# Kernel optimization log

Hardware: AMD Instinct MI355X
Metric: run time of the kernel (lower is better)

## Reference

```python
import jax, jax.numpy as jnp
import numpy as np

HOP = 2
N_NODES = 50000
D_FEAT = 64
N_NNZ = 800000
N_QEDGES = 32768


def setup_inputs() -> dict:
    key = jax.random.key(0)
    k1, k2, k3, k4, k5 = jax.random.split(key, 5)
    x = jax.random.normal(k1, (N_NODES, D_FEAT), dtype=jnp.float32)
    # degrees must be strictly positive (reciprocal / rsqrt / sqrt applied)
    deg = 1.0 + 63.0 * jax.random.uniform(k2, (N_NODES, 1), dtype=jnp.float32)
    adj_row = jnp.sort(jax.random.randint(k3, (N_NNZ,), 0, N_NODES, dtype=jnp.int32))
    adj_col = jax.random.randint(k4, (N_NNZ,), 0, N_NODES, dtype=jnp.int32)
    edge = jax.random.randint(k5, (2, N_QEDGES), 0, N_NODES, dtype=jnp.int32)
    return {"x": x, "deg": deg, "adj_row": adj_row, "adj_col": adj_col, "edge": edge}


def reference(x, deg, adj_row, adj_col, edge):
    N, D = x.shape
    degrev = 1.0 / deg                      # [N,1]
    # fused degree feature expansion: [N, 3D]
    x3 = jnp.concatenate((x, x * jax.lax.rsqrt(deg), x * jnp.sqrt(deg)), axis=1)

    def spmm(v):  # unweighted adj_t @ v via gather + segment-sum
        return jax.ops.segment_sum(v[adj_col], adj_row, num_segments=N)

    xs = [x3, degrev * spmm(x3)]
    for _ in range(2, HOP + 1):  # Chebyshev-like recurrence
        xs.append(degrev * spmm(xs[-1]) - xs[-2])
    h = jnp.concatenate(xs, axis=1)              # [N, (hop+1)*3*D]
    h = h.reshape(N, 3 * (HOP + 1), D)           # unflatten(1, (-1, D))
    h = jnp.transpose(h, (0, 2, 1))              # [N, D, 3*(hop+1)]
    return h[edge]                               # [2, E_q, D, 3*(hop+1)]
```

## Files before the change

kernel.cpp:

```cpp
#include <hip/hip_runtime.h>

#define N_NODES 50000
#define D_FEAT 64
#define N_NNZ 800000
#define N_ENT 65536

__global__ void build_rowptr_scal(const int* __restrict__ adj_row,
                                  const float* __restrict__ deg,
                                  int* __restrict__ row_ptr,
                                  float4* __restrict__ scal,
                                  int nnz, int n) {
    int r = blockIdx.x * blockDim.x + threadIdx.x;
    if (r > n) return;
    int lo = 0, hi = nnz;
    while (lo < hi) {
        int mid = (lo + hi) >> 1;
        if (adj_row[mid] < r) lo = mid + 1; else hi = mid;
    }
    row_ptr[r] = lo;
    if (r < n) {
        float d  = deg[r];
        float sq = sqrtf(d);
        scal[r] = make_float4(1.0f / d, 1.0f / sq, sq, 0.0f);
    }
}

__global__ __launch_bounds__(256) void spmm1_kernel(
    const float4* __restrict__ x4, const float4* __restrict__ scal,
    const int* __restrict__ adj_col, const int* __restrict__ row_ptr,
    float4* __restrict__ y1, int n) {
    int wave = threadIdx.x >> 6;
    int t    = threadIdx.x & 63;
    int sub  = t >> 4;
    int f    = t & 15;
    int r    = blockIdx.x * 4 + wave;
    if (r >= n) return;

    int s = row_ptr[r], e = row_ptr[r + 1];
    int cnt = e - s;
    float4 a0 = make_float4(0.f, 0.f, 0.f, 0.f), a1 = a0, a2 = a0;

    int nfull = cnt & ~3;
#pragma unroll 2
    for (int i = 0; i < nfull; i += 4) {
        int c = adj_col[s + i + sub];
        float4 sc = scal[c];
        float4 xv = x4[(size_t)c * 16 + f];
        a0.x += xv.x;        a0.y += xv.y;        a0.z += xv.z;        a0.w += xv.w;
        a1.x += xv.x * sc.y; a1.y += xv.y * sc.y; a1.z += xv.z * sc.y; a1.w += xv.w * sc.y;
        a2.x += xv.x * sc.z; a2.y += xv.y * sc.z; a2.z += xv.z * sc.z; a2.w += xv.w * sc.z;
    }
    if (nfull + sub < cnt) {
        int c = adj_col[s + nfull + sub];
        float4 sc = scal[c];
        float4 xv = x4[(size_t)c * 16 + f];
        a0.x += xv.x;        a0.y += xv.y;        a0.z += xv.z;        a0.w += xv.w;
        a1.x += xv.x * sc.y; a1.y += xv.y * sc.y; a1.z += xv.z * sc.y; a1.w += xv.w * sc.y;
        a2.x += xv.x * sc.z; a2.y += xv.y * sc.z; a2.z += xv.z * sc.z; a2.w += xv.w * sc.z;
    }

#pragma unroll
    for (int off = 16; off <= 32; off <<= 1) {
        a0.x += __shfl_xor(a0.x, off); a0.y += __shfl_xor(a0.y, off);
        a0.z += __shfl_xor(a0.z, off); a0.w += __shfl_xor(a0.w, off);
        a1.x += __shfl_xor(a1.x, off); a1.y += __shfl_xor(a1.y, off);
        a1.z += __shfl_xor(a1.z, off); a1.w += __shfl_xor(a1.w, off);
        a2.x += __shfl_xor(a2.x, off); a2.y += __shfl_xor(a2.y, off);
        a2.z += __shfl_xor(a2.z, off); a2.w += __shfl_xor(a2.w, off);
    }

    float dr = scal[r].x;
    if (sub < 3) {
        float4 res = (sub == 0) ? a0 : (sub == 1) ? a1 : a2;
        res.x *= dr; res.y *= dr; res.z *= dr; res.w *= dr;
        y1[(size_t)r * 48 + sub * 16 + f] = res;
    }
}

__global__ __launch_bounds__(256) void spmm2_kernel(
    const float4* __restrict__ x4, const float4* __restrict__ scal,
    const int* __restrict__ adj_col, const int* __restrict__ row_ptr,
    const float4* __restrict__ y1, float4* __restrict__ y2, int n) {
    int wave = threadIdx.x >> 6;
    int t    = threadIdx.x & 63;
    int sub  = t >> 4;
    int f    = t & 15;
    int r    = blockIdx.x * 4 + wave;
    if (r >= n) return;

    int s = row_ptr[r], e = row_ptr[r + 1];
    int cnt = e - s;
    float4 a0 = make_float4(0.f, 0.f, 0.f, 0.f), a1 = a0, a2 = a0;

    int nfull = cnt & ~3;
#pragma unroll 2
    for (int i = 0; i < nfull; i += 4) {
        int c = adj_col[s + i + sub];
        const float4* yc = y1 + (size_t)c * 48;
        float4 b0 = yc[f], b1 = yc[16 + f], b2 = yc[32 + f];
        a0.x += b0.x; a0.y += b0.y; a0.z += b0.z; a0.w += b0.w;
        a1.x += b1.x; a1.y += b1.y; a1.z += b1.z; a1.w += b1.w;
        a2.x += b2.x; a2.y += b2.y; a2.z += b2.z; a2.w += b2.w;
    }
    if (nfull + sub < cnt) {
        int c = adj_col[s + nfull + sub];
        const float4* yc = y1 + (size_t)c * 48;
        float4 b0 = yc[f], b1 = yc[16 + f], b2 = yc[32 + f];
        a0.x += b0.x; a0.y += b0.y; a0.z += b0.z; a0.w += b0.w;
        a1.x += b1.x; a1.y += b1.y; a1.z += b1.z; a1.w += b1.w;
        a2.x += b2.x; a2.y += b2.y; a2.z += b2.z; a2.w += b2.w;
    }

#pragma unroll
    for (int off = 16; off <= 32; off <<= 1) {
        a0.x += __shfl_xor(a0.x, off); a0.y += __shfl_xor(a0.y, off);
        a0.z += __shfl_xor(a0.z, off); a0.w += __shfl_xor(a0.w, off);
        a1.x += __shfl_xor(a1.x, off); a1.y += __shfl_xor(a1.y, off);
        a1.z += __shfl_xor(a1.z, off); a1.w += __shfl_xor(a1.w, off);
        a2.x += __shfl_xor(a2.x, off); a2.y += __shfl_xor(a2.y, off);
        a2.z += __shfl_xor(a2.z, off); a2.w += __shfl_xor(a2.w, off);
    }

    float4 sc = scal[r];
    float4 xv = x4[(size_t)r * 16 + f];
    if (sub < 3) {
        float4 res = (sub == 0) ? a0 : (sub == 1) ? a1 : a2;
        float w = (sub == 0) ? 1.0f : (sub == 1) ? sc.y : sc.z;
        res.x = sc.x * res.x - xv.x * w;
        res.y = sc.x * res.y - xv.y * w;
        res.z = sc.x * res.z - xv.z * w;
        res.w = sc.x * res.w - xv.w * w;
        y2[(size_t)r * 48 + sub * 16 + f] = res;
    }
}

__global__ __launch_bounds__(256) void gather_kernel(
    const float* __restrict__ x, const float4* __restrict__ scal,
    const int* __restrict__ edge, const float* __restrict__ y1,
    const float* __restrict__ y2, float* __restrict__ out) {
    __shared__ __align__(16) float lds[4][576];
    int wave = threadIdx.x >> 6;
    int t    = threadIdx.x & 63;
    int ent  = blockIdx.x * 4 + wave;

    int n = edge[ent];
    float4 sc = scal[n];
    float xv = x[n * D_FEAT + t];
    const float* y1n = y1 + (size_t)n * 192;
    const float* y2n = y2 + (size_t)n * 192;

    float h[9];
    h[0] = xv;          h[1] = xv * sc.y;   h[2] = xv * sc.z;
    h[3] = y1n[t];      h[4] = y1n[64 + t]; h[5] = y1n[128 + t];
    h[6] = y2n[t];      h[7] = y2n[64 + t]; h[8] = y2n[128 + t];

#pragma unroll
    for (int g = 0; g < 9; ++g) lds[wave][t * 9 + g] = h[g];
    __syncthreads();

    const float4* l4 = (const float4*)lds[wave];
    float4* o4 = (float4*)(out + (size_t)ent * 576);
    o4[t]      = l4[t];
    o4[t + 64] = l4[t + 64];
    if (t < 16) o4[t + 128] = l4[t + 128];
}

extern "C" void kernel_launch(void* const* d_in, const int* in_sizes, int n_in,
                              void* d_out, int out_size, void* d_ws, size_t ws_size,
                              hipStream_t stream) {
    const float* x       = (const float*)d_in[0];
    const float* deg     = (const float*)d_in[1];
    const int*   adj_row = (const int*)d_in[2];
    const int*   adj_col = (const int*)d_in[3];
    const int*   edge    = (const int*)d_in[4];
    float* out = (float*)d_out;

    char* ws = (char*)d_ws;
    size_t off = 0;
    int*    row_ptr = (int*)ws;      off = ((size_t)(N_NODES + 1) * 4 + 255) & ~(size_t)255;
    float4* scal    = (float4*)(ws + off); off += (size_t)N_NODES * 16;
    off = (off + 255) & ~(size_t)255;
    float4* y1      = (float4*)(ws + off); off += (size_t)N_NODES * 192 * 4;
    float4* y2      = (float4*)(ws + off);

    const float4* x4 = (const float4*)x;

    build_rowptr_scal<<<(N_NODES + 1 + 255) / 256, 256, 0, stream>>>(
        adj_row, deg, row_ptr, scal, N_NNZ, N_NODES);
    spmm1_kernel<<<(N_NODES + 3) / 4, 256, 0, stream>>>(
        x4, scal, adj_col, row_ptr, y1, N_NODES);
    spmm2_kernel<<<(N_NODES + 3) / 4, 256, 0, stream>>>(
        x4, scal, adj_col, row_ptr, y1, y2, N_NODES);
    gather_kernel<<<N_ENT / 4, 256, 0, stream>>>(
        x, scal, edge, (const float*)y1, (const float*)y2, out);
}
```

Before: 310.6 us.

## Store x and intermediate hop features as bf16 to halve gather traffic

Adds a pack_x kernel that converts x to bf16 and stores the spmm1/spmm2 outputs y1/y2 as bf16 with round-to-nearest-even, while accumulating in fp32. Each lane now loads 8 bf16 features per 16-byte load, so the spmm kernels process 8 neighbors per wave iteration instead of 4. The aim is to cut the memory traffic of the random neighbor gathers and of the final edge gather. The cost is an extra pack kernel and lower precision in the intermediate and output values, which may exceed the tolerance.

```diff
diff --git a/kernel.cpp b/kernel.cpp
--- a/kernel.cpp
+++ b/kernel.cpp
@@ -4,6 +4,26 @@
 #define D_FEAT 64
 #define N_NNZ 800000
 #define N_ENT 65536
+
+typedef unsigned int uint32;
+typedef unsigned short ushort16;
+
+__device__ __forceinline__ uint32 rne1(float a) {
+    uint32 u = __float_as_uint(a);
+    return (u + 0x7FFFu + ((u >> 16) & 1u)) >> 16;
+}
+__device__ __forceinline__ uint32 rne2(float a, float b) {
+    return rne1(a) | (rne1(b) << 16);
+}
+__device__ __forceinline__ float bf_lo(uint32 u) { return __uint_as_float(u << 16); }
+__device__ __forceinline__ float bf_hi(uint32 u) { return __uint_as_float(u & 0xFFFF0000u); }
+__device__ __forceinline__ void unpack8(const uint4 v, float* f) {
+    f[0] = bf_lo(v.x); f[1] = bf_hi(v.x);
+    f[2] = bf_lo(v.y); f[3] = bf_hi(v.y);
+    f[4] = bf_lo(v.z); f[5] = bf_hi(v.z);
+    f[6] = bf_lo(v.w); f[7] = bf_hi(v.w);
+}
+__device__ __forceinline__ float bf1(ushort16 u) { return __uint_as_float(((uint32)u) << 16); }
 
 __global__ void build_rowptr_scal(const int* __restrict__ adj_row,
                                   const float* __restrict__ deg,
@@ -25,119 +45,148 @@
     }
 }
 
+__global__ __launch_bounds__(256) void pack_x(const float2* __restrict__ x2,
+                                              uint32* __restrict__ xh, int npair) {
+    int i = blockIdx.x * blockDim.x + threadIdx.x;
+    if (i >= npair) return;
+    float2 v = x2[i];
+    xh[i] = rne2(v.x, v.y);
+}
+
 __global__ __launch_bounds__(256) void spmm1_kernel(
-    const float4* __restrict__ x4, const float4* __restrict__ scal,
+    const uint4* __restrict__ xh, const float4* __restrict__ scal,
     const int* __restrict__ adj_col, const int* __restrict__ row_ptr,
-    float4* __restrict__ y1, int n) {
+    uint4* __restrict__ y1h, int n) {
     int wave = threadIdx.x >> 6;
     int t    = threadIdx.x & 63;
-    int sub  = t >> 4;
-    int f    = t & 15;
+    int sub  = t >> 3;
+    int f    = t & 7;
     int r    = blockIdx.x * 4 + wave;
     if (r >= n) return;
 
     int s = row_ptr[r], e = row_ptr[r + 1];
     int cnt = e - s;
-    float4 a0 = make_float4(0.f, 0.f, 0.f, 0.f), a1 = a0, a2 = a0;
-
-    int nfull = cnt & ~3;
-#pragma unroll 2
-    for (int i = 0; i < nfull; i += 4) {
+    float acc[3][8];
+#pragma unroll
+    for (int g = 0; g < 3; ++g)
+#pragma unroll
+        for (int j = 0; j < 8; ++j) acc[g][j] = 0.f;
+
+    int nfull = cnt & ~7;
+    for (int i = 0; i < nfull; i += 8) {
         int c = adj_col[s + i + sub];
         float4 sc = scal[c];
-        float4 xv = x4[(size_t)c * 16 + f];
-        a0.x += xv.x;        a0.y += xv.y;        a0.z += xv.z;        a0.w += xv.w;
-        a1.x += xv.x * sc.y; a1.y += xv.y * sc.y; a1.z += xv.z * sc.y; a1.w += xv.w * sc.y;
-        a2.x += xv.x * sc.z; a2.y += xv.y * sc.z; a2.z += xv.z * sc.z; a2.w += xv.w * sc.z;
+        uint4 xv = xh[(size_t)c * 8 + f];
+        float xf[8]; unpack8(xv, xf);
+#pragma unroll
+        for (int j = 0; j < 8; ++j) {
+            acc[0][j] += xf[j];
+            acc[1][j] += xf[j] * sc.y;
+            acc[2][j] += xf[j] * sc.z;
+        }
     }
     if (nfull + sub < cnt) {
         int c = adj_col[s + nfull + sub];
         float4 sc = scal[c];
-        float4 xv = x4[(size_t)c * 16 + f];
-        a0.x += xv.x;        a0.y += xv.y;        a0.z += xv.z;        a0.w += xv.w;
-        a1.x += xv.x * sc.y; a1.y += xv.y * sc.y; a1.z += xv.z * sc.y; a1.w += xv.w * sc.y;
-        a2.x += xv.x * sc.z; a2.y += xv.y * sc.z; a2.z += xv.z * sc.z; a2.w += xv.w * sc.z;
-    }
-
-#pragma unroll
-    for (int off = 16; off <= 32; off <<= 1) {
-        a0.x += __shfl_xor(a0.x, off); a0.y += __shfl_xor(a0.y, off);
-        a0.z += __shfl_xor(a0.z, off); a0.w += __shfl_xor(a0.w, off);
-        a1.x += __shfl_xor(a1.x, off); a1.y += __shfl_xor(a1.y, off);
-        a1.z += __shfl_xor(a1.z, off); a1.w += __shfl_xor(a1.w, off);
-        a2.x += __shfl_xor(a2.x, off); a2.y += __shfl_xor(a2.y, off);
-        a2.z += __shfl_xor(a2.z, off); a2.w += __shfl_xor(a2.w, off);
-    }
+        uint4 xv = xh[(size_t)c * 8 + f];
+        float xf[8]; unpack8(xv, xf);
+#pragma unroll
+        for (int j = 0; j < 8; ++j) {
+            acc[0][j] += xf[j];
+            acc[1][j] += xf[j] * sc.y;
+            acc[2][j] += xf[j] * sc.z;
+        }
+    }
+
+#pragma unroll
+    for (int off = 8; off <= 32; off <<= 1)
+#pragma unroll
+        for (int g = 0; g < 3; ++g)
+#pragma unroll
+            for (int j = 0; j < 8; ++j)
+                acc[g][j] += __shfl_xor(acc[g][j], off);
 
     float dr = scal[r].x;
     if (sub < 3) {
-        float4 res = (sub == 0) ? a0 : (sub == 1) ? a1 : a2;
-        res.x *= dr; res.y *= dr; res.z *= dr; res.w *= dr;
-        y1[(size_t)r * 48 + sub * 16 + f] = res;
+        float v[8];
+#pragma unroll
+        for (int j = 0; j < 8; ++j) v[j] = acc[sub][j] * dr;
+        uint4 o = make_uint4(rne2(v[0], v[1]), rne2(v[2], v[3]),
+                             rne2(v[4], v[5]), rne2(v[6], v[7]));
+        y1h[(size_t)r * 24 + sub * 8 + f] = o;
     }
 }
 
 __global__ __launch_bounds__(256) void spmm2_kernel(
     const float4* __restrict__ x4, const float4* __restrict__ scal,
     const int* __restrict__ adj_col, const int* __restrict__ row_ptr,
-    const float4* __restrict__ y1, float4* __restrict__ y2, int n) {
+    const uint4* __restrict__ y1h, uint4* __restrict__ y2h, int n) {
     int wave = threadIdx.x >> 6;
     int t    = threadIdx.x & 63;
-    int sub  = t >> 4;
-    int f    = t & 15;
+    int sub  = t >> 3;
+    int f    = t & 7;
     int r    = blockIdx.x * 4 + wave;
     if (r >= n) return;
 
     int s = row_ptr[r], e = row_ptr[r + 1];
     int cnt = e - s;
-    float4 a0 = make_float4(0.f, 0.f, 0.f, 0.f), a1 = a0, a2 = a0;
-
-    int nfull = cnt & ~3;
-#pragma unroll 2
-    for (int i = 0; i < nfull; i += 4) {
+    float acc[3][8];
+#pragma unroll
+    for (int g = 0; g < 3; ++g)
+#pragma unroll
+        for (int j = 0; j < 8; ++j) acc[g][j] = 0.f;
+
+    int nfull = cnt & ~7;
+    for (int i = 0; i < nfull; i += 8) {
         int c = adj_col[s + i + sub];
-        const float4* yc = y1 + (size_t)c * 48;
-        float4 b0 = yc[f], b1 = yc[16 + f], b2 = yc[32 + f];
-        a0.x += b0.x; a0.y += b0.y; a0.z += b0.z; a0.w += b0.w;
-        a1.x += b1.x; a1.y += b1.y; a1.z += b1.z; a1.w += b1.w;
-        a2.x += b2.x; a2.y += b2.y; a2.z += b2.z; a2.w += b2.w;
+        const uint4* yc = y1h + (size_t)c * 24;
+        uint4 b0 = yc[f], b1 = yc[8 + f], b2 = yc[16 + f];
+        float f0[8], f1[8], f2[8];
+        unpack8(b0, f0); unpack8(b1, f1); unpack8(b2, f2);
+#pragma unroll
+        for (int j = 0; j < 8; ++j) {
+            acc[0][j] += f0[j]; acc[1][j] += f1[j]; acc[2][j] += f2[j];
+        }
     }
     if (nfull + sub < cnt) {
         int c = adj_col[s + nfull + sub];
-        const float4* yc = y1 + (size_t)c * 48;
-        float4 b0 = yc[f], b1 = yc[16 + f], b2 = yc[32 + f];
-        a0.x += b0.x; a0.y += b0.y; a0.z += b0.z; a0.w += b0.w;
-        a1.x += b1.x; a1.y += b1.y; a1.z += b1.z; a1.w += b1.w;
-        a2.x += b2.x; a2.y += b2.y; a2.z += b2.z; a2.w += b2.w;
-    }
-
-#pragma unroll
-    for (int off = 16; off <= 32; off <<= 1) {
-        a0.x += __shfl_xor(a0.x, off); a0.y += __shfl_xor(a0.y, off);
-        a0.z += __shfl_xor(a0.z, off); a0.w += __shfl_xor(a0.w, off);
-        a1.x += __shfl_xor(a1.x, off); a1.y += __shfl_xor(a1.y, off);
-        a1.z += __shfl_xor(a1.z, off); a1.w += __shfl_xor(a1.w, off);
-        a2.x += __shfl_xor(a2.x, off); a2.y += __shfl_xor(a2.y, off);
-        a2.z += __shfl_xor(a2.z, off); a2.w += __shfl_xor(a2.w, off);
-    }
+        const uint4* yc = y1h + (size_t)c * 24;
+        uint4 b0 = yc[f], b1 = yc[8 + f], b2 = yc[16 + f];
+        float f0[8], f1[8], f2[8];
+        unpack8(b0, f0); unpack8(b1, f1); unpack8(b2, f2);
+#pragma unroll
+        for (int j = 0; j < 8; ++j) {
+            acc[0][j] += f0[j]; acc[1][j] += f1[j]; acc[2][j] += f2[j];
+        }
+    }
+
+#pragma unroll
+    for (int off = 8; off <= 32; off <<= 1)
+#pragma unroll
+        for (int g = 0; g < 3; ++g)
+#pragma unroll
+            for (int j = 0; j < 8; ++j)
+                acc[g][j] += __shfl_xor(acc[g][j], off);
 
     float4 sc = scal[r];
-    float4 xv = x4[(size_t)r * 16 + f];
     if (sub < 3) {
-        float4 res = (sub == 0) ? a0 : (sub == 1) ? a1 : a2;
         float w = (sub == 0) ? 1.0f : (sub == 1) ? sc.y : sc.z;
-        res.x = sc.x * res.x - xv.x * w;
-        res.y = sc.x * res.y - xv.y * w;
-        res.z = sc.x * res.z - xv.z * w;
-        res.w = sc.x * res.w - xv.w * w;
-        y2[(size_t)r * 48 + sub * 16 + f] = res;
+        float4 xa = x4[(size_t)r * 16 + f * 2];
+        float4 xb = x4[(size_t)r * 16 + f * 2 + 1];
+        float xr[8] = {xa.x, xa.y, xa.z, xa.w, xb.x, xb.y, xb.z, xb.w};
+        float v[8];
+#pragma unroll
+        for (int j = 0; j < 8; ++j) v[j] = sc.x * acc[sub][j] - xr[j] * w;
+        uint4 o = make_uint4(rne2(v[0], v[1]), rne2(v[2], v[3]),
+                             rne2(v[4], v[5]), rne2(v[6], v[7]));
+        y2h[(size_t)r * 24 + sub * 8 + f] = o;
     }
 }
 
 __global__ __launch_bounds__(256) void gather_kernel(
     const float* __restrict__ x, const float4* __restrict__ scal,
-    const int* __restrict__ edge, const float* __restrict__ y1,
-    const float* __restrict__ y2, float* __restrict__ out) {
+    const int* __restrict__ edge, const ushort16* __restrict__ y1h,
+    const ushort16* __restrict__ y2h, float* __restrict__ out) {
     __shared__ __align__(16) float lds[4][576];
     int wave = threadIdx.x >> 6;
     int t    = threadIdx.x & 63;
@@ -146,13 +195,13 @@
     int n = edge[ent];
     float4 sc = scal[n];
     float xv = x[n * D_FEAT + t];
-    const float* y1n = y1 + (size_t)n * 192;
-    const float* y2n = y2 + (size_t)n * 192;
+    const ushort16* y1n = y1h + (size_t)n * 192;
+    const ushort16* y2n = y2h + (size_t)n * 192;
 
     float h[9];
-    h[0] = xv;          h[1] = xv * sc.y;   h[2] = xv * sc.z;
-    h[3] = y1n[t];      h[4] = y1n[64 + t]; h[5] = y1n[128 + t];
-    h[6] = y2n[t];      h[7] = y2n[64 + t]; h[8] = y2n[128 + t];
+    h[0] = xv;              h[1] = xv * sc.y;       h[2] = xv * sc.z;
+    h[3] = bf1(y1n[t]);     h[4] = bf1(y1n[64 + t]); h[5] = bf1(y1n[128 + t]);
+    h[6] = bf1(y2n[t]);     h[7] = bf1(y2n[64 + t]); h[8] = bf1(y2n[128 + t]);
 
 #pragma unroll
     for (int g = 0; g < 9; ++g) lds[wave][t * 9 + g] = h[g];
@@ -177,20 +226,22 @@
 
     char* ws = (char*)d_ws;
     size_t off = 0;
-    int*    row_ptr = (int*)ws;      off = ((size_t)(N_NODES + 1) * 4 + 255) & ~(size_t)255;
+    int*    row_ptr = (int*)ws;            off = ((size_t)(N_NODES + 1) * 4 + 255) & ~(size_t)255;
     float4* scal    = (float4*)(ws + off); off += (size_t)N_NODES * 16;
+    uint32* xh      = (uint32*)(ws + off); off += (size_t)N_NODES * 64 * 2;
     off = (off + 255) & ~(size_t)255;
-    float4* y1      = (float4*)(ws + off); off += (size_t)N_NODES * 192 * 4;
-    float4* y2      = (float4*)(ws + off);
-
-    const float4* x4 = (const float4*)x;
+    uint4*  y1h     = (uint4*)(ws + off);  off += (size_t)N_NODES * 192 * 2;
+    off = (off + 255) & ~(size_t)255;
+    uint4*  y2h     = (uint4*)(ws + off);
 
     build_rowptr_scal<<<(N_NODES + 1 + 255) / 256, 256, 0, stream>>>(
         adj_row, deg, row_ptr, scal, N_NNZ, N_NODES);
+    pack_x<<<(N_NODES * 32 + 255) / 256, 256, 0, stream>>>(
+        (const float2*)x, xh, N_NODES * 32);
     spmm1_kernel<<<(N_NODES + 3) / 4, 256, 0, stream>>>(
-        x4, scal, adj_col, row_ptr, y1, N_NODES);
+        (const uint4*)xh, scal, adj_col, row_ptr, y1h, N_NODES);
     spmm2_kernel<<<(N_NODES + 3) / 4, 256, 0, stream>>>(
-        x4, scal, adj_col, row_ptr, y1, y2, N_NODES);
+        (const float4*)x, scal, adj_col, row_ptr, y1h, y2h, N_NODES);
     gather_kernel<<<N_ENT / 4, 256, 0, stream>>>(
-        x, scal, edge, (const float*)y1, (const float*)y2, out);
-}
+        x, scal, edge, (const ushort16*)y1h, (const ushort16*)y2h, out);
+}
```

Result: faster. 296.0 us (-4.7%).
